# Kernel tuning notes

Measured on AMD Instinct MI355X. Metric: run time of the kernel, lower is better.

The kernel has to match this reference:

```python
import jax, jax.numpy as jnp
import numpy as np

BATCH, FIELD_DIM, EMBED_DIM = 4096, 20000, 64


def setup_inputs() -> dict:
    key = jax.random.key(0)
    k_idx, k_w = jax.random.split(key)
    # multi-hot indicator matrix (values in {0,1})
    indices = jax.random.randint(k_idx, (BATCH, FIELD_DIM), 0, 2, dtype=jnp.int32)
    # kaiming_normal_ on (field_dim, embed_dim): std = sqrt(2 / fan_in), fan_in = embed_dim
    W = jax.random.normal(k_w, (FIELD_DIM, EMBED_DIM), dtype=jnp.float32) * np.sqrt(2.0 / EMBED_DIM)
    return {"indices": indices, "W": W}


def reference(indices, W):
    # Per row: gather embeddings at nonzero positions and sum ('sum' aggregate).
    # Equivalent to binary-mask @ W; rows with no nonzeros yield zeros naturally.
    mask = (indices != 0).astype(W.dtype)          # [B, F]
    out = jnp.einsum('bf,fd->bd', mask, W)         # [B, D]
    return out
```

## Files before the change

### kernel.cpp

```cpp
#include <hip/hip_runtime.h>
#include <hip/hip_bf16.h>

#define BATCH 4096
#define FIELD 20000
#define EMBED 64
#define KSTEPS 625
#define KC     25
#define SPW    25
#define MTILES 256
#define TOTAL_WAVES (MTILES * KC)
#define WSWZ_DWORDS (FIELD * EMBED / 2)
#define PART_STRIDE (MTILES * 1024)

typedef __attribute__((ext_vector_type(4))) float  f32x4;
typedef __attribute__((ext_vector_type(8))) short  short8;
typedef __attribute__((ext_vector_type(4))) int    i32x4;
typedef __attribute__((ext_vector_type(4))) unsigned int u32x4;

__device__ __forceinline__ unsigned bf16_rtne(float f) {
    unsigned u = __builtin_bit_cast(unsigned, f);
    return (u + 0x7FFFu + ((u >> 16) & 1u)) >> 16;
}

__global__ __launch_bounds__(256) void prep_w_kernel(const float* __restrict__ W,
                                                     unsigned int* __restrict__ Wswz) {
    __shared__ float lds[32 * 65];
    const int t  = threadIdx.x;
    const int s0 = blockIdx.x;

    const float4* src = (const float4*)(W + (size_t)s0 * 2048);
    float4 a = src[t * 2 + 0];
    float4 b = src[t * 2 + 1];
    int l  = t * 8;
    int kl = l >> 6, c = l & 63;
    float* dst = lds + kl * 65 + c;
    dst[0] = a.x; dst[1] = a.y; dst[2] = a.z; dst[3] = a.w;
    dst[4] = b.x; dst[5] = b.y; dst[6] = b.z; dst[7] = b.w;
    __syncthreads();

    const int lane = t & 63, tq = t >> 6;
    const int khi = lane >> 4, lrow = lane & 15;
    const int col = tq * 16 + lrow;
    u32x4 o;
#pragma unroll
    for (int j2 = 0; j2 < 4; ++j2) {
        int kloc = khi * 8 + 2 * j2;
        float w0 = lds[kloc * 65 + col];
        float w1 = lds[(kloc + 1) * 65 + col];
        o[j2] = bf16_rtne(w0) | (bf16_rtne(w1) << 16);
    }
    *(u32x4*)(Wswz + ((size_t)(s0 * 4 + tq) * 64 + lane) * 4) = o;
}

__global__ __launch_bounds__(256) void emb_mfma_kernel(const int* __restrict__ idxm,
                                                       const unsigned int* __restrict__ Wswz,
                                                       float* __restrict__ P) {
    const int lane  = threadIdx.x & 63;
    const int w     = blockIdx.x * 4 + (threadIdx.x >> 6);
    const int mtile = w % MTILES;
    const int kc    = w / MTILES;
    const int lrow  = lane & 15;
    const int khi   = lane >> 4;
    const int row   = mtile * 16 + lrow;

    const i32x4* pA = (const i32x4*)(idxm + (size_t)row * FIELD
                                     + (size_t)kc * SPW * 32 + khi * 8);
    const short8* pB = (const short8*)Wswz + (size_t)kc * SPW * 4 * 64 + lane;

    f32x4 acc0 = {0.f, 0.f, 0.f, 0.f};
    f32x4 acc1 = acc0, acc2 = acc0, acc3 = acc0;

#pragma unroll 5
    for (int s = 0; s < SPW; ++s) {
        i32x4 x = pA[0];
        i32x4 y = pA[1];
        pA += 8;

        unsigned m0 = (x.x != 0 ? 0x3F80u : 0u) | (x.y != 0 ? 0x3F800000u : 0u);
        unsigned m1 = (x.z != 0 ? 0x3F80u : 0u) | (x.w != 0 ? 0x3F800000u : 0u);
        unsigned m2 = (y.x != 0 ? 0x3F80u : 0u) | (y.y != 0 ? 0x3F800000u : 0u);
        unsigned m3 = (y.z != 0 ? 0x3F80u : 0u) | (y.w != 0 ? 0x3F800000u : 0u);
        u32x4 av = {m0, m1, m2, m3};
        short8 afrag = __builtin_bit_cast(short8, av);

        short8 b0 = pB[0];
        short8 b1 = pB[64];
        short8 b2 = pB[128];
        short8 b3 = pB[192];
        pB += 256;

        acc0 = __builtin_amdgcn_mfma_f32_16x16x32_bf16(afrag, b0, acc0, 0, 0, 0);
        acc1 = __builtin_amdgcn_mfma_f32_16x16x32_bf16(afrag, b1, acc1, 0, 0, 0);
        acc2 = __builtin_amdgcn_mfma_f32_16x16x32_bf16(afrag, b2, acc2, 0, 0, 0);
        acc3 = __builtin_amdgcn_mfma_f32_16x16x32_bf16(afrag, b3, acc3, 0, 0, 0);
    }

    float* pP = P + (size_t)(kc * MTILES + mtile) * 1024 + lane * 4;
    *(f32x4*)(pP + 0)   = acc0;
    *(f32x4*)(pP + 256) = acc1;
    *(f32x4*)(pP + 512) = acc2;
    *(f32x4*)(pP + 768) = acc3;
}

__global__ __launch_bounds__(256) void reduce_kernel(const float* __restrict__ P,
                                                     float* __restrict__ out) {
    const int tid = blockIdx.x * 256 + threadIdx.x;
    float s = 0.f;
#pragma unroll
    for (int kc = 0; kc < KC; ++kc)
        s += P[(size_t)kc * PART_STRIDE + tid];

    const int i     = tid & 3;
    const int lane  = (tid >> 2) & 63;
    const int f     = (tid >> 8) & 3;
    const int mtile = tid >> 10;
    const int row   = mtile * 16 + (lane >> 4) * 4 + i;
    const int col   = f * 16 + (lane & 15);
    out[(size_t)row * EMBED + col] = s;
}

extern "C" void kernel_launch(void* const* d_in, const int* in_sizes, int n_in,
                              void* d_out, int out_size, void* d_ws, size_t ws_size,
                              hipStream_t stream) {
    const int*   idxm = (const int*)d_in[0];
    const float* W    = (const float*)d_in[1];
    float*       out  = (float*)d_out;

    unsigned int* Wswz = (unsigned int*)d_ws;
    float*        P    = (float*)((char*)d_ws + (size_t)WSWZ_DWORDS * 4);

    hipLaunchKernelGGL(prep_w_kernel, dim3(KSTEPS), dim3(256), 0, stream, W, Wswz);
    hipLaunchKernelGGL(emb_mfma_kernel, dim3(TOTAL_WAVES / 4), dim3(256), 0, stream,
                       idxm, Wswz, P);
    hipLaunchKernelGGL(reduce_kernel, dim3(BATCH * EMBED / 256), dim3(256), 0, stream,
                       P, out);
}
```

Measured before the change: 106.1 us.

## Coalesce index loads via ballot bitmasks in LDS and atomically reduce partials

Each wave now reads its 16 rows of the indicator matrix with fully coalesced per-row loads. It packs the nonzero tests into bitmasks with ballots and stores them in shared memory, then builds the bf16 A fragments from those bits inside the MFMA loop. The separate partial-sum buffer and reduction kernel are removed: the W-prep kernel zeroes the output, and each wave atomically adds its accumulators into the output. This is meant to improve memory access efficiency on the dominant 328MB index read and to remove one launch and the partial buffer traffic. In exchange it adds float atomics, which make the summation order nondeterministic, plus extra ballot and LDS work.

```diff
diff --git a/kernel.cpp b/kernel.cpp
--- a/kernel.cpp
+++ b/kernel.cpp
@@ -4,18 +4,17 @@
 #define BATCH 4096
 #define FIELD 20000
 #define EMBED 64
-#define KSTEPS 625
 #define KC     25
+#define KSPAN  800
 #define SPW    25
 #define MTILES 256
-#define TOTAL_WAVES (MTILES * KC)
-#define WSWZ_DWORDS (FIELD * EMBED / 2)
-#define PART_STRIDE (MTILES * 1024)
+#define LROW_STRIDE 26
+#define WAVE_LDS (16 * LROW_STRIDE)
 
 typedef __attribute__((ext_vector_type(4))) float  f32x4;
 typedef __attribute__((ext_vector_type(8))) short  short8;
-typedef __attribute__((ext_vector_type(4))) int    i32x4;
 typedef __attribute__((ext_vector_type(4))) unsigned int u32x4;
+typedef unsigned long long u64;
 
 __device__ __forceinline__ unsigned bf16_rtne(float f) {
     unsigned u = __builtin_bit_cast(unsigned, f);
@@ -23,7 +22,13 @@
 }
 
 __global__ __launch_bounds__(256) void prep_w_kernel(const float* __restrict__ W,
-                                                     unsigned int* __restrict__ Wswz) {
+                                                     unsigned int* __restrict__ Wswz,
+                                                     float* __restrict__ out) {
+    if (blockIdx.x < 512) {
+        float2 z; z.x = 0.f; z.y = 0.f;
+        ((float2*)out)[blockIdx.x * 256 + threadIdx.x] = z;
+    }
+
     __shared__ float lds[32 * 65];
     const int t  = threadIdx.x;
     const int s0 = blockIdx.x;
@@ -54,40 +59,55 @@
 
 __global__ __launch_bounds__(256) void emb_mfma_kernel(const int* __restrict__ idxm,
                                                        const unsigned int* __restrict__ Wswz,
-                                                       float* __restrict__ P) {
+                                                       float* __restrict__ out) {
+    __shared__ unsigned lmask[4 * WAVE_LDS];
     const int lane  = threadIdx.x & 63;
-    const int w     = blockIdx.x * 4 + (threadIdx.x >> 6);
+    const int widx  = threadIdx.x >> 6;
+    const int w     = blockIdx.x * 4 + widx;
     const int mtile = w % MTILES;
     const int kc    = w / MTILES;
     const int lrow  = lane & 15;
     const int khi   = lane >> 4;
-    const int row   = mtile * 16 + lrow;
+    unsigned* lm = lmask + widx * WAVE_LDS;
 
-    const i32x4* pA = (const i32x4*)(idxm + (size_t)row * FIELD
-                                     + (size_t)kc * SPW * 32 + khi * 8);
+    for (int r = 0; r < 16; ++r) {
+        const int* rp = idxm + (size_t)(mtile * 16 + r) * FIELD + kc * KSPAN;
+        int v[13];
+#pragma unroll
+        for (int c = 0; c < 12; ++c) v[c] = rp[c * 64 + lane];
+        v[12] = 1;
+        if (lane < 32) v[12] = rp[768 + lane];
+#pragma unroll
+        for (int c = 0; c < 12; ++c) {
+            u64 b = __ballot(v[c] != 0);
+            if (lane == 0)
+                *(u64*)&lm[r * LROW_STRIDE + 2 * c] = b;
+        }
+        u64 bt = __ballot(v[12] != 0);
+        if (lane == 0)
+            lm[r * LROW_STRIDE + 24] = (unsigned)bt;
+    }
+    __syncthreads();
+
     const short8* pB = (const short8*)Wswz + (size_t)kc * SPW * 4 * 64 + lane;
+    const unsigned* mrow = lm + lrow * LROW_STRIDE;
 
     f32x4 acc0 = {0.f, 0.f, 0.f, 0.f};
     f32x4 acc1 = acc0, acc2 = acc0, acc3 = acc0;
 
 #pragma unroll 5
     for (int s = 0; s < SPW; ++s) {
-        i32x4 x = pA[0];
-        i32x4 y = pA[1];
-        pA += 8;
+        unsigned Mw = mrow[s];
+        short8 b0 = pB[0], b1 = pB[64], b2 = pB[128], b3 = pB[192];
+        pB += 256;
 
-        unsigned m0 = (x.x != 0 ? 0x3F80u : 0u) | (x.y != 0 ? 0x3F800000u : 0u);
-        unsigned m1 = (x.z != 0 ? 0x3F80u : 0u) | (x.w != 0 ? 0x3F800000u : 0u);
-        unsigned m2 = (y.x != 0 ? 0x3F80u : 0u) | (y.y != 0 ? 0x3F800000u : 0u);
-        unsigned m3 = (y.z != 0 ? 0x3F80u : 0u) | (y.w != 0 ? 0x3F800000u : 0u);
-        u32x4 av = {m0, m1, m2, m3};
+        unsigned mb = Mw >> (khi * 8);
+        u32x4 av;
+#pragma unroll
+        for (int j = 0; j < 4; ++j)
+            av[j] = (((mb >> (2 * j)) & 1u) ? 0x3F80u : 0u)
+                  | (((mb >> (2 * j + 1)) & 1u) ? 0x3F800000u : 0u);
         short8 afrag = __builtin_bit_cast(short8, av);
-
-        short8 b0 = pB[0];
-        short8 b1 = pB[64];
-        short8 b2 = pB[128];
-        short8 b3 = pB[192];
-        pB += 256;
 
         acc0 = __builtin_amdgcn_mfma_f32_16x16x32_bf16(afrag, b0, acc0, 0, 0, 0);
         acc1 = __builtin_amdgcn_mfma_f32_16x16x32_bf16(afrag, b1, acc1, 0, 0, 0);
@@ -95,28 +115,15 @@
         acc3 = __builtin_amdgcn_mfma_f32_16x16x32_bf16(afrag, b3, acc3, 0, 0, 0);
     }
 
-    float* pP = P + (size_t)(kc * MTILES + mtile) * 1024 + lane * 4;
-    *(f32x4*)(pP + 0)   = acc0;
-    *(f32x4*)(pP + 256) = acc1;
-    *(f32x4*)(pP + 512) = acc2;
-    *(f32x4*)(pP + 768) = acc3;
-}
-
-__global__ __launch_bounds__(256) void reduce_kernel(const float* __restrict__ P,
-                                                     float* __restrict__ out) {
-    const int tid = blockIdx.x * 256 + threadIdx.x;
-    float s = 0.f;
+    float* obase = out + (size_t)mtile * 16 * EMBED;
 #pragma unroll
-    for (int kc = 0; kc < KC; ++kc)
-        s += P[(size_t)kc * PART_STRIDE + tid];
-
-    const int i     = tid & 3;
-    const int lane  = (tid >> 2) & 63;
-    const int f     = (tid >> 8) & 3;
-    const int mtile = tid >> 10;
-    const int row   = mtile * 16 + (lane >> 4) * 4 + i;
-    const int col   = f * 16 + (lane & 15);
-    out[(size_t)row * EMBED + col] = s;
+    for (int i = 0; i < 4; ++i) {
+        int orow = khi * 4 + i;
+        atomicAdd(obase + (size_t)orow * EMBED +      lrow, acc0[i]);
+        atomicAdd(obase + (size_t)orow * EMBED + 16 + lrow, acc1[i]);
+        atomicAdd(obase + (size_t)orow * EMBED + 32 + lrow, acc2[i]);
+        atomicAdd(obase + (size_t)orow * EMBED + 48 + lrow, acc3[i]);
+    }
 }
 
 extern "C" void kernel_launch(void* const* d_in, const int* in_sizes, int n_in,
@@ -125,13 +132,10 @@
     const int*   idxm = (const int*)d_in[0];
     const float* W    = (const float*)d_in[1];
     float*       out  = (float*)d_out;
+    unsigned int* Wswz = (unsigned int*)d_ws;
 
-    unsigned int* Wswz = (unsigned int*)d_ws;
-    float*        P    = (float*)((char*)d_ws + (size_t)WSWZ_DWORDS * 4);
-
-    hipLaunchKernelGGL(prep_w_kernel, dim3(KSTEPS), dim3(256), 0, stream, W, Wswz);
-    hipLaunchKernelGGL(emb_mfma_kernel, dim3(TOTAL_WAVES / 4), dim3(256), 0, stream,
-                       idxm, Wswz, P);
-    hipLaunchKernelGGL(reduce_kernel, dim3(BATCH * EMBED / 256), dim3(256), 0, stream,
-                       P, out);
+    hipLaunchKernelGGL(prep_w_kernel, dim3(FIELD / 32), dim3(256), 0, stream,
+                       W, Wswz, out);
+    hipLaunchKernelGGL(emb_mfma_kernel, dim3(MTILES * KC / 4), dim3(256), 0, stream,
+                       idxm, Wswz, out);
 }
```

Result: faster. 90.11 us (-15.1%).
